# Optimization experiments

Hardware: AMD Instinct MI355X
Metric: run time of the kernel (lower is better)

Reference implementation:

```python
import jax, jax.numpy as jnp
import numpy as np

N = 16384        # number of nodes
F_IN = 128       # dim_nodes
H = 128          # hidden_channels
OUT = 2


def setup_inputs() -> dict:
    key = jax.random.key(0)
    ks = jax.random.split(key, 8)
    x = jax.random.normal(ks[0], (N, F_IN), dtype=jnp.float32)
    adjacency = jax.random.uniform(ks[1], (N, N), dtype=jnp.float32)
    # GCNConv weights (aggregate then linear) and final head
    w1 = jax.random.normal(ks[2], (F_IN, H), dtype=jnp.float32) / np.sqrt(F_IN)
    b1 = jnp.zeros((H,), dtype=jnp.float32)
    w2 = jax.random.normal(ks[3], (H, H), dtype=jnp.float32) / np.sqrt(H)
    b2 = jnp.zeros((H,), dtype=jnp.float32)
    w3 = jax.random.normal(ks[4], (H, OUT), dtype=jnp.float32) / np.sqrt(H)
    b3 = jnp.zeros((OUT,), dtype=jnp.float32)
    return {"x": x, "adjacency": adjacency, "w1": w1, "b1": b1,
            "w2": w2, "b2": b2, "w3": w3, "b3": b3}


def reference(x, adjacency, w1, b1, w2, b2, w3, b3):
    # GCNConv layer 1: adjacency aggregation + linear, then ReLU
    h = jax.nn.relu(adjacency @ (x @ w1) + b1)      # [N, H]
    # GCNConv layer 2
    h = jax.nn.relu(adjacency @ (h @ w2) + b2)      # [N, H]
    # dropout p=0.5 is identity at inference (training=False)
    # Linear head -> 2 classes
    return h @ w3 + b3                              # [N, 2]
```

## Files before the change

kernel.cpp:

```cpp
#include <hip/hip_runtime.h>

typedef __bf16 bf16_t;
typedef __bf16 bf16x8 __attribute__((ext_vector_type(8)));
typedef __bf16 bf16x4 __attribute__((ext_vector_type(4)));
typedef float f32x4 __attribute__((ext_vector_type(4)));

constexpr int NN = 16384;
constexpr int F  = 128;
constexpr int BM = 64;
constexpr int BK = 64;
constexpr int LDA = 72;
constexpr int LDB = 72;
constexpr int SPLITK = 4;
constexpr int KSPAN  = NN / SPLITK;

template<bool IN_BF16>
__global__ __launch_bounds__(256)
void small_gemm_T(const void* __restrict__ inp, const float* __restrict__ w,
                  bf16_t* __restrict__ outT)
{
    __shared__ float xt[32 * 132];
    const int t  = threadIdx.x;
    const int i0 = blockIdx.x * 32;
    {
        const int r = t >> 3, cc = (t & 7) * 16;
        float* dst = &xt[r * 132 + cc];
        if constexpr (!IN_BF16) {
            const float* src = (const float*)inp + (size_t)(i0 + r) * F + cc;
            float4 v0 = ((const float4*)src)[0];
            float4 v1 = ((const float4*)src)[1];
            float4 v2 = ((const float4*)src)[2];
            float4 v3 = ((const float4*)src)[3];
            ((float4*)dst)[0] = v0; ((float4*)dst)[1] = v1;
            ((float4*)dst)[2] = v2; ((float4*)dst)[3] = v3;
        } else {
            const bf16_t* src = (const bf16_t*)inp + (size_t)(i0 + r) * F + cc;
            bf16x8 v0 = ((const bf16x8*)src)[0];
            bf16x8 v1 = ((const bf16x8*)src)[1];
            #pragma unroll
            for (int q = 0; q < 8; q++) { dst[q] = (float)v0[q]; dst[8 + q] = (float)v1[q]; }
        }
    }
    __syncthreads();
    const int j  = t & 127;
    const int r0 = (t >> 7) * 16;
    float acc[16];
    #pragma unroll
    for (int r = 0; r < 16; r++) acc[r] = 0.f;
    for (int k4 = 0; k4 < F / 4; k4++) {
        const float w0 = w[(k4 * 4 + 0) * F + j];
        const float w1v = w[(k4 * 4 + 1) * F + j];
        const float w2v = w[(k4 * 4 + 2) * F + j];
        const float w3v = w[(k4 * 4 + 3) * F + j];
        #pragma unroll
        for (int r = 0; r < 16; r++) {
            const float4 xv = *(const float4*)&xt[(r0 + r) * 132 + k4 * 4];
            acc[r] += xv.x * w0 + xv.y * w1v + xv.z * w2v + xv.w * w3v;
        }
    }
    bf16_t* dst = outT + (size_t)j * NN + i0 + r0;
    #pragma unroll
    for (int r = 0; r < 16; r++) dst[r] = (bf16_t)acc[r];
}

__global__ __launch_bounds__(256, 4)
void agg_gemm_split(const float* __restrict__ Aadj, const bf16_t* __restrict__ BT,
                    float* __restrict__ Ppart)
{
    __shared__ bf16_t sA[BM * LDA];
    __shared__ bf16_t sB[F * LDB];
    const int t = threadIdx.x;
    const int m0 = blockIdx.x * BM;
    const int kq = blockIdx.y;
    const int kbeg = kq * KSPAN;
    const int kend = kbeg + KSPAN;
    const int w = t >> 6, lane = t & 63, quad = lane >> 4, l16 = lane & 15;

    f32x4 acc[4][2];
    #pragma unroll
    for (int mf = 0; mf < 4; mf++)
        #pragma unroll
        for (int nf = 0; nf < 2; nf++) acc[mf][nf] = (f32x4){0.f, 0.f, 0.f, 0.f};

    const int am = t >> 2, ac = (t & 3) * 16;
    const float* aptr = Aadj + (size_t)(m0 + am) * NN + ac;
    bf16_t* sA_dst = &sA[am * LDA + ac];
    const int bn = t >> 1, bc = (t & 1) * 32;
    const bf16_t* bptr = BT + (size_t)bn * NN + bc;
    bf16_t* sB_dst = &sB[bn * LDB + bc];

    f32x4 av[4];
    bf16x8 bv[4];
    {
        const f32x4* ap = (const f32x4*)(aptr + kbeg);
        av[0] = __builtin_nontemporal_load(ap + 0);
        av[1] = __builtin_nontemporal_load(ap + 1);
        av[2] = __builtin_nontemporal_load(ap + 2);
        av[3] = __builtin_nontemporal_load(ap + 3);
        const bf16x8* bp = (const bf16x8*)(bptr + kbeg);
        bv[0] = bp[0]; bv[1] = bp[1]; bv[2] = bp[2]; bv[3] = bp[3];
    }

    for (int k0 = kbeg; k0 < kend; k0 += BK) {
        {
            bf16x8 p0, p1;
            const float* fs = (const float*)av;
            #pragma unroll
            for (int q = 0; q < 8; q++) { p0[q] = (bf16_t)fs[q]; p1[q] = (bf16_t)fs[8 + q]; }
            ((bf16x8*)sA_dst)[0] = p0; ((bf16x8*)sA_dst)[1] = p1;
            ((bf16x8*)sB_dst)[0] = bv[0]; ((bf16x8*)sB_dst)[1] = bv[1];
            ((bf16x8*)sB_dst)[2] = bv[2]; ((bf16x8*)sB_dst)[3] = bv[3];
        }
        __syncthreads();
        {
            const int kn = (k0 + BK < kend) ? (k0 + BK) : kbeg;
            const f32x4* ap = (const f32x4*)(aptr + kn);
            av[0] = __builtin_nontemporal_load(ap + 0);
            av[1] = __builtin_nontemporal_load(ap + 1);
            av[2] = __builtin_nontemporal_load(ap + 2);
            av[3] = __builtin_nontemporal_load(ap + 3);
            const bf16x8* bp = (const bf16x8*)(bptr + kn);
            bv[0] = bp[0]; bv[1] = bp[1]; bv[2] = bp[2]; bv[3] = bp[3];
        }
        #pragma unroll
        for (int ks = 0; ks < 2; ks++) {
            bf16x8 afr[4], bfr[2];
            #pragma unroll
            for (int mf = 0; mf < 4; mf++)
                afr[mf] = *(const bf16x8*)&sA[(mf * 16 + l16) * LDA + ks * 32 + quad * 8];
            #pragma unroll
            for (int nf = 0; nf < 2; nf++)
                bfr[nf] = *(const bf16x8*)&sB[(w * 32 + nf * 16 + l16) * LDB + ks * 32 + quad * 8];
            #pragma unroll
            for (int mf = 0; mf < 4; mf++)
                #pragma unroll
                for (int nf = 0; nf < 2; nf++)
                    acc[mf][nf] = __builtin_amdgcn_mfma_f32_16x16x32_bf16(
                        afr[mf], bfr[nf], acc[mf][nf], 0, 0, 0);
        }
        __syncthreads();
    }

    float* dst = Ppart + (size_t)kq * NN * F;
    #pragma unroll
    for (int mf = 0; mf < 4; mf++)
        #pragma unroll
        for (int nf = 0; nf < 2; nf++) {
            const int col = w * 32 + nf * 16 + l16;
            #pragma unroll
            for (int r = 0; r < 4; r++) {
                const int row = m0 + mf * 16 + quad * 4 + r;
                dst[(size_t)row * F + col] = acc[mf][nf][r];
            }
        }
}

__global__ __launch_bounds__(256)
void finish_h(const float* __restrict__ P, const float* __restrict__ bias,
              bf16_t* __restrict__ h)
{
    const int g = blockIdx.x * 256 + threadIdx.x;
    const int row = g >> 5;
    const int c4  = g & 31;
    const size_t off = (size_t)row * F + c4 * 4;
    f32x4 s = *(const f32x4*)(P + off);
    #pragma unroll
    for (int kq = 1; kq < SPLITK; kq++)
        s += *(const f32x4*)(P + (size_t)kq * NN * F + off);
    const f32x4 b = *(const f32x4*)(bias + c4 * 4);
    bf16x4 o;
    #pragma unroll
    for (int q = 0; q < 4; q++) {
        float v = s[q] + b[q];
        o[q] = (bf16_t)(v > 0.f ? v : 0.f);
    }
    *(bf16x4*)(h + off) = o;
}

__global__ __launch_bounds__(256)
void finish_final(const float* __restrict__ P, const float* __restrict__ b2,
                  const float* __restrict__ w3, const float* __restrict__ b3,
                  float* __restrict__ out)
{
    const int t = threadIdx.x, w = t >> 6, l = t & 63;
    const int base = blockIdx.x * 64;
    const float w00 = w3[l * 2],        w01 = w3[l * 2 + 1];
    const float w10 = w3[(l + 64) * 2], w11 = w3[(l + 64) * 2 + 1];
    const float bb0 = b2[l], bb1 = b2[l + 64];
    const float o0 = b3[0], o1 = b3[1];
    for (int rr = 0; rr < 16; rr++) {
        const int row = base + rr * 4 + w;
        const float* p = P + (size_t)row * F;
        float v0 = p[l], v1 = p[l + 64];
        #pragma unroll
        for (int kq = 1; kq < SPLITK; kq++) {
            const float* pk = p + (size_t)kq * NN * F;
            v0 += pk[l]; v1 += pk[l + 64];
        }
        v0 += bb0; v1 += bb1;
        v0 = v0 > 0.f ? v0 : 0.f;
        v1 = v1 > 0.f ? v1 : 0.f;
        float p0 = v0 * w00 + v1 * w10;
        float p1 = v0 * w01 + v1 * w11;
        #pragma unroll
        for (int off = 32; off > 0; off >>= 1) {
            p0 += __shfl_down(p0, off);
            p1 += __shfl_down(p1, off);
        }
        if (l == 0) {
            out[(size_t)row * 2 + 0] = p0 + o0;
            out[(size_t)row * 2 + 1] = p1 + o1;
        }
    }
}

extern "C" void kernel_launch(void* const* d_in, const int* in_sizes, int n_in,
                              void* d_out, int out_size, void* d_ws, size_t ws_size,
                              hipStream_t stream)
{
    const float* x   = (const float*)d_in[0];
    const float* adj = (const float*)d_in[1];
    const float* w1  = (const float*)d_in[2];
    const float* b1  = (const float*)d_in[3];
    const float* w2  = (const float*)d_in[4];
    const float* b2  = (const float*)d_in[5];
    const float* w3  = (const float*)d_in[6];
    const float* b3  = (const float*)d_in[7];
    float* out = (float*)d_out;

    bf16_t* xw1T  = (bf16_t*)d_ws;
    bf16_t* h1    = xw1T + (size_t)F * NN;
    bf16_t* hw2T  = h1   + (size_t)NN * F;
    float*  Ppart = (float*)(hw2T + (size_t)F * NN);

    dim3 agrid(NN / BM, SPLITK);

    small_gemm_T<false><<<NN / 32, 256, 0, stream>>>((const void*)x, w1, xw1T);
    agg_gemm_split<<<agrid, 256, 0, stream>>>(adj, xw1T, Ppart);
    finish_h<<<NN * F / 4 / 256, 256, 0, stream>>>(Ppart, b1, h1);
    small_gemm_T<true><<<NN / 32, 256, 0, stream>>>((const void*)h1, w2, hw2T);
    agg_gemm_split<<<agrid, 256, 0, stream>>>(adj, hw2T, Ppart);
    finish_final<<<NN / 64, 256, 0, stream>>>(Ppart, b2, w3, b3, out);
}
```

Baseline: 1.960 ms.

## Pre-convert adjacency to bf16 and use direct-to-LDS loads in aggregation GEMM

Adds a pass that converts the fp32 adjacency matrix to bf16 once in workspace, so both aggregation GEMMs read half the bytes and skip per-tile conversion in registers. The aggregation kernel is rewritten to 128x128 tiles with 2x2 wave layout. It loads tiles with global_load_lds into an XOR-swizzled LDS layout to avoid bank conflicts, and uses a block-id swizzle. Split-K is raised to 8. In exchange it adds a 1 GB read plus 512 MB write conversion pass, a much larger workspace, and a single-buffered main loop with no register prefetch.

```diff
diff --git a/kernel.cpp b/kernel.cpp
--- a/kernel.cpp
+++ b/kernel.cpp
@@ -7,12 +7,23 @@
 
 constexpr int NN = 16384;
 constexpr int F  = 128;
-constexpr int BM = 64;
 constexpr int BK = 64;
-constexpr int LDA = 72;
-constexpr int LDB = 72;
-constexpr int SPLITK = 4;
+constexpr int SPLITK = 8;
 constexpr int KSPAN  = NN / SPLITK;
+
+__global__ __launch_bounds__(256)
+void convert_adj(const float* __restrict__ a, bf16_t* __restrict__ o)
+{
+    const size_t total4 = (size_t)NN * NN / 4;
+    const size_t stride = (size_t)gridDim.x * 256;
+    for (size_t i = (size_t)blockIdx.x * 256 + threadIdx.x; i < total4; i += stride) {
+        f32x4 v = *(const f32x4*)(a + i * 4);
+        bf16x4 p;
+        #pragma unroll
+        for (int q = 0; q < 4; q++) p[q] = (bf16_t)v[q];
+        *(bf16x4*)(o + i * 4) = p;
+    }
+}
 
 template<bool IN_BF16>
 __global__ __launch_bounds__(256)
@@ -63,78 +74,59 @@
     for (int r = 0; r < 16; r++) dst[r] = (bf16_t)acc[r];
 }
 
-__global__ __launch_bounds__(256, 4)
-void agg_gemm_split(const float* __restrict__ Aadj, const bf16_t* __restrict__ BT,
-                    float* __restrict__ Ppart)
-{
-    __shared__ bf16_t sA[BM * LDA];
-    __shared__ bf16_t sB[F * LDB];
+__global__ __launch_bounds__(256)
+void agg_mm(const bf16_t* __restrict__ Abf, const bf16_t* __restrict__ BT,
+            float* __restrict__ Ppart)
+{
+    __shared__ bf16_t sA[128 * 64];
+    __shared__ bf16_t sB[128 * 64];
     const int t = threadIdx.x;
-    const int m0 = blockIdx.x * BM;
-    const int kq = blockIdx.y;
+    const int bid = blockIdx.x;
+    const int swz = (bid & 7) * 128 + (bid >> 3);
+    const int kq  = swz >> 7;
+    const int m0  = (swz & 127) * 128;
     const int kbeg = kq * KSPAN;
-    const int kend = kbeg + KSPAN;
-    const int w = t >> 6, lane = t & 63, quad = lane >> 4, l16 = lane & 15;
-
-    f32x4 acc[4][2];
-    #pragma unroll
-    for (int mf = 0; mf < 4; mf++)
-        #pragma unroll
-        for (int nf = 0; nf < 2; nf++) acc[mf][nf] = (f32x4){0.f, 0.f, 0.f, 0.f};
-
-    const int am = t >> 2, ac = (t & 3) * 16;
-    const float* aptr = Aadj + (size_t)(m0 + am) * NN + ac;
-    bf16_t* sA_dst = &sA[am * LDA + ac];
-    const int bn = t >> 1, bc = (t & 1) * 32;
-    const bf16_t* bptr = BT + (size_t)bn * NN + bc;
-    bf16_t* sB_dst = &sB[bn * LDB + bc];
-
-    f32x4 av[4];
-    bf16x8 bv[4];
-    {
-        const f32x4* ap = (const f32x4*)(aptr + kbeg);
-        av[0] = __builtin_nontemporal_load(ap + 0);
-        av[1] = __builtin_nontemporal_load(ap + 1);
-        av[2] = __builtin_nontemporal_load(ap + 2);
-        av[3] = __builtin_nontemporal_load(ap + 3);
-        const bf16x8* bp = (const bf16x8*)(bptr + kbeg);
-        bv[0] = bp[0]; bv[1] = bp[1]; bv[2] = bp[2]; bv[3] = bp[3];
-    }
-
-    for (int k0 = kbeg; k0 < kend; k0 += BK) {
-        {
-            bf16x8 p0, p1;
-            const float* fs = (const float*)av;
-            #pragma unroll
-            for (int q = 0; q < 8; q++) { p0[q] = (bf16_t)fs[q]; p1[q] = (bf16_t)fs[8 + q]; }
-            ((bf16x8*)sA_dst)[0] = p0; ((bf16x8*)sA_dst)[1] = p1;
-            ((bf16x8*)sB_dst)[0] = bv[0]; ((bf16x8*)sB_dst)[1] = bv[1];
-            ((bf16x8*)sB_dst)[2] = bv[2]; ((bf16x8*)sB_dst)[3] = bv[3];
-        }
+    const int w = t >> 6, lane = t & 63;
+    const int quad = lane >> 4, l16 = lane & 15;
+    const int wr = w >> 1, wc = w & 1;
+
+    f32x4 acc[4][4];
+    #pragma unroll
+    for (int i = 0; i < 4; i++)
+        #pragma unroll
+        for (int j = 0; j < 4; j++) acc[i][j] = (f32x4){0.f, 0.f, 0.f, 0.f};
+
+    const int srow8 = lane >> 3;
+    const int sc8   = (lane & 7) ^ srow8;
+    const bf16_t* abase = Abf + (size_t)(m0 + w * 32 + srow8) * NN + sc8 * 8;
+    const bf16_t* bbase = BT  + (size_t)(w * 32 + srow8) * NN + sc8 * 8;
+
+    for (int k0 = kbeg; k0 < kbeg + KSPAN; k0 += BK) {
+        #pragma unroll
+        for (int c = 0; c < 4; c++)
+            __builtin_amdgcn_global_load_lds(
+                (const unsigned int*)(abase + (size_t)(c * 8) * NN + k0),
+                (unsigned int*)&sA[(w * 32 + c * 8) * 64], 16, 0, 0);
+        #pragma unroll
+        for (int c = 0; c < 4; c++)
+            __builtin_amdgcn_global_load_lds(
+                (const unsigned int*)(bbase + (size_t)(c * 8) * NN + k0),
+                (unsigned int*)&sB[(w * 32 + c * 8) * 64], 16, 0, 0);
         __syncthreads();
-        {
-            const int kn = (k0 + BK < kend) ? (k0 + BK) : kbeg;
-            const f32x4* ap = (const f32x4*)(aptr + kn);
-            av[0] = __builtin_nontemporal_load(ap + 0);
-            av[1] = __builtin_nontemporal_load(ap + 1);
-            av[2] = __builtin_nontemporal_load(ap + 2);
-            av[3] = __builtin_nontemporal_load(ap + 3);
-            const bf16x8* bp = (const bf16x8*)(bptr + kn);
-            bv[0] = bp[0]; bv[1] = bp[1]; bv[2] = bp[2]; bv[3] = bp[3];
-        }
         #pragma unroll
         for (int ks = 0; ks < 2; ks++) {
-            bf16x8 afr[4], bfr[2];
+            const int cst = (((ks * 4 + quad) ^ (l16 & 7)) * 8);
+            bf16x8 afr[4], bfr[4];
             #pragma unroll
             for (int mf = 0; mf < 4; mf++)
-                afr[mf] = *(const bf16x8*)&sA[(mf * 16 + l16) * LDA + ks * 32 + quad * 8];
-            #pragma unroll
-            for (int nf = 0; nf < 2; nf++)
-                bfr[nf] = *(const bf16x8*)&sB[(w * 32 + nf * 16 + l16) * LDB + ks * 32 + quad * 8];
+                afr[mf] = *(const bf16x8*)&sA[(wr * 64 + mf * 16 + l16) * 64 + cst];
+            #pragma unroll
+            for (int nf = 0; nf < 4; nf++)
+                bfr[nf] = *(const bf16x8*)&sB[(wc * 64 + nf * 16 + l16) * 64 + cst];
             #pragma unroll
             for (int mf = 0; mf < 4; mf++)
                 #pragma unroll
-                for (int nf = 0; nf < 2; nf++)
+                for (int nf = 0; nf < 4; nf++)
                     acc[mf][nf] = __builtin_amdgcn_mfma_f32_16x16x32_bf16(
                         afr[mf], bfr[nf], acc[mf][nf], 0, 0, 0);
         }
@@ -145,11 +137,11 @@
     #pragma unroll
     for (int mf = 0; mf < 4; mf++)
         #pragma unroll
-        for (int nf = 0; nf < 2; nf++) {
-            const int col = w * 32 + nf * 16 + l16;
+        for (int nf = 0; nf < 4; nf++) {
+            const int col = wc * 64 + nf * 16 + l16;
             #pragma unroll
             for (int r = 0; r < 4; r++) {
-                const int row = m0 + mf * 16 + quad * 4 + r;
+                const int row = m0 + wr * 64 + mf * 16 + quad * 4 + r;
                 dst[(size_t)row * F + col] = acc[mf][nf][r];
             }
         }
@@ -228,17 +220,17 @@
     const float* b3  = (const float*)d_in[7];
     float* out = (float*)d_out;
 
-    bf16_t* xw1T  = (bf16_t*)d_ws;
-    bf16_t* h1    = xw1T + (size_t)F * NN;
-    bf16_t* hw2T  = h1   + (size_t)NN * F;
+    bf16_t* Abf  = (bf16_t*)d_ws;
+    bf16_t* xw1T = Abf  + (size_t)NN * NN;
+    bf16_t* h1   = xw1T + (size_t)F * NN;
+    bf16_t* hw2T = h1   + (size_t)NN * F;
     float*  Ppart = (float*)(hw2T + (size_t)F * NN);
 
-    dim3 agrid(NN / BM, SPLITK);
-
+    convert_adj<<<2048, 256, 0, stream>>>(adj, Abf);
     small_gemm_T<false><<<NN / 32, 256, 0, stream>>>((const void*)x, w1, xw1T);
-    agg_gemm_split<<<agrid, 256, 0, stream>>>(adj, xw1T, Ppart);
+    agg_mm<<<128 * SPLITK, 256, 0, stream>>>(Abf, xw1T, Ppart);
     finish_h<<<NN * F / 4 / 256, 256, 0, stream>>>(Ppart, b1, h1);
     small_gemm_T<true><<<NN / 32, 256, 0, stream>>>((const void*)h1, w2, hw2T);
-    agg_gemm_split<<<agrid, 256, 0, stream>>>(adj, hw2T, Ppart);
+    agg_mm<<<128 * SPLITK, 256, 0, stream>>>(Abf, hw2T, Ppart);
     finish_final<<<NN / 64, 256, 0, stream>>>(Ppart, b2, w3, b3, out);
 }
```

Result: faster. 1.851 ms (-5.6%).
